# Kernel optimization log

Measured on AMD Instinct MI355X. Metric: run time of the kernel, lower is better.

The kernel has to match this reference:

```python
import jax, jax.numpy as jnp
import numpy as np

BATCH = 2048
SEQ_LEN = 8192


def setup_inputs() -> dict:
    key = jax.random.key(0)
    k1, k2 = jax.random.split(key)
    inputs = jax.random.normal(k1, (BATCH, SEQ_LEN), dtype=jnp.float32)
    filters = jax.random.normal(k2, (BATCH, SEQ_LEN), dtype=jnp.float32)
    return {"inputs": inputs, "filters": filters}


def reference(inputs, filters):
    # FFT-based long convolution with zero-padding to 2L (linear, not circular, conv).
    # torch norm='forward': rfft divides by n, irfft multiplies by n -> net scale 1/n.
    L = inputs.shape[-1]
    n = 2 * L  # rfft with n=2L implicitly zero-pads, same as F.pad then rfft
    x_f = jnp.fft.rfft(inputs, n=n, axis=-1, norm="forward")   # (B, L+1) complex
    h_f = jnp.fft.rfft(filters, n=n, axis=-1, norm="forward")  # (B, L+1) complex
    y = jnp.fft.irfft(x_f * h_f, n=n, axis=-1, norm="forward")  # (B, 2L)
    return y[..., :L]
```

## Files before the change

kernel.cpp:

```cpp
#include <hip/hip_runtime.h>

#define L_LEN 8192
#define N_FFT 16384
#define NB    1024

#define LB __launch_bounds__(NB)

typedef float f2 __attribute__((ext_vector_type(2)));

__device__ __forceinline__ f2 mkf2(float a, float b) { f2 v; v.x = a; v.y = b; return v; }

__device__ __forceinline__ f2 cmul(f2 a, f2 w) {
    return mkf2(a.y, a.y) * mkf2(-w.y, w.x) + mkf2(a.x, a.x) * w;
}

__device__ __forceinline__ void sincos_rev(float rev, float* sn, float* cs) {
    *sn = __builtin_amdgcn_sinf(rev);
    *cs = __builtin_amdgcn_cosf(rev);
}

__host__ __device__ constexpr int swz(int i) {
    return i ^ ((((i) >> 4) ^ ((i) >> 8) ^ ((i) >> 12)) & 15);
}

__device__ __forceinline__ int rev4_12(int m) {
    int r = 0;
#pragma unroll
    for (int d = 0; d < 6; ++d) { r = (r << 2) | (m & 3); m >>= 2; }
    return r;
}

__device__ __forceinline__ void bfly_dif(f2& x0, f2& x1, f2& x2, f2& x3,
                                         f2 w1, f2 w2, f2 w3) {
    f2 A = x0 + x2, B = x0 - x2, C = x1 + x3, D = x1 - x3;
    f2 iD = mkf2(-D.y, D.x);
    x0 = A + C;
    x1 = cmul(B - iD, w1);
    x2 = cmul(A - C, w2);
    x3 = cmul(B + iD, w3);
}

__device__ __forceinline__ void bfly_dit(f2& x0, f2& x1, f2& x2, f2& x3,
                                         f2 w1, f2 w2, f2 w3) {
    f2 a1 = cmul(x1, w1), a2 = cmul(x2, w2), a3 = cmul(x3, w3);
    f2 E = x0 + a2, F = x0 - a2, G = a1 + a3, K = a1 - a3;
    f2 iK = mkf2(-K.y, K.x);
    x0 = E + G; x1 = F + iK; x2 = E - G; x3 = F - iK;
}

__device__ __forceinline__ void bfly_dif1(f2* z) {
    f2 A = z[0] + z[2], B = z[0] - z[2], C = z[1] + z[3], D = z[1] - z[3];
    f2 iD = mkf2(-D.y, D.x);
    z[0] = A + C; z[1] = B - iD; z[2] = A - C; z[3] = B + iD;
}
__device__ __forceinline__ void bfly_dit1(f2* z) {
    f2 E = z[0] + z[2], F = z[0] - z[2], G = z[1] + z[3], K = z[1] - z[3];
    f2 iK = mkf2(-K.y, K.x);
    z[0] = E + G; z[1] = F + iK; z[2] = E - G; z[3] = F - iK;
}

__device__ __forceinline__ void pointwise_pair(f2& Zm, f2& Zr) {
    f2 half = mkf2(0.5f, 0.5f);
    f2 X = half * (Zm + mkf2(Zr.x, -Zr.y));
    f2 H = half * (mkf2(Zm.y, -Zm.x) + mkf2(Zr.y, Zr.x));
    f2 Y = cmul(X, H);
    Zm = Y;
    Zr = mkf2(Y.x, -Y.y);
}

#define CT0 1.0f
#define CT1 0.92387953251128674f
#define CT2 0.70710678118654752f
#define CT3 0.38268343236508977f
#define ST1 0.38268343236508977f
#define ST2 0.70710678118654752f
#define ST3 0.92387953251128674f

__device__ __forceinline__ void fwd_first(f2* lds, int tid,
                                          const float* __restrict__ xr,
                                          const float* __restrict__ hr) {
    f2 r[4][4];
    float snA, csA;
    sincos_rev((float)tid * (-1.0f / 16384.f), &snA, &csA);
    f2 u1 = mkf2(csA, snA);
    const f2 lad[4] = {mkf2(CT0, 0.f), mkf2(CT1, -ST1), mkf2(CT2, -ST2), mkf2(CT3, -ST3)};
#pragma unroll
    for (int jB = 0; jB < 4; ++jB) {
        const int t = tid + jB * 1024;
        f2 z0 = mkf2(xr[t], hr[t]);
        f2 z1 = mkf2(xr[t + 4096], hr[t + 4096]);
        f2 w1 = (jB == 0) ? u1 : cmul(u1, lad[jB]);
        f2 w2 = cmul(w1, w1);
        f2 w3 = cmul(w2, w1);
        f2 iz1 = mkf2(-z1.y, z1.x);
        r[0][jB] = z0 + z1;
        r[1][jB] = cmul(z0 - iz1, w1);
        r[2][jB] = cmul(z0 - z1, w2);
        r[3][jB] = cmul(z0 + iz1, w3);
    }
    float sn, cs;
    sincos_rev((float)tid * (-1.0f / 4096.f), &sn, &cs);
    f2 v1 = mkf2(cs, sn);
    f2 v2 = cmul(v1, v1);
    f2 v3 = cmul(v2, v1);
#pragma unroll
    for (int jA = 0; jA < 4; ++jA)
        bfly_dif(r[jA][0], r[jA][1], r[jA][2], r[jA][3], v1, v2, v3);

    const int sb = swz(tid);
#pragma unroll
    for (int jA = 0; jA < 4; ++jA)
#pragma unroll
        for (int jB = 0; jB < 4; ++jB)
            lds[sb ^ swz(jA * 4096 + jB * 1024)] = r[jA][jB];
}

__device__ __forceinline__ void inv_last(const f2* lds, int tid,
                                         float* __restrict__ orow) {
    const int sb = swz(tid);
    f2 r[4][4];
#pragma unroll
    for (int jA = 0; jA < 4; ++jA)
#pragma unroll
        for (int jB = 0; jB < 4; ++jB)
            r[jA][jB] = lds[sb ^ swz(jA * 1024 + jB * 4096)];

    {
        float sn, cs;
        sincos_rev((float)tid * (1.0f / 4096.f), &sn, &cs);
        f2 a1 = mkf2(cs, sn);
        f2 a2 = cmul(a1, a1);
        f2 a3 = cmul(a2, a1);
#pragma unroll
        for (int jB = 0; jB < 4; ++jB)
            bfly_dit(r[0][jB], r[1][jB], r[2][jB], r[3][jB], a1, a2, a3);
    }
    const float scale = 1.0f / ((float)N_FFT * (float)N_FFT);
    float sn, cs;
    sincos_rev((float)tid * (1.0f / 16384.f), &sn, &cs);
    f2 b1 = mkf2(cs, sn);
    const f2 lad[4] = {mkf2(CT0, 0.f), mkf2(CT1, ST1), mkf2(CT2, ST2), mkf2(CT3, ST3)};
#pragma unroll
    for (int jA = 0; jA < 4; ++jA) {
        f2 w1 = (jA == 0) ? b1 : cmul(b1, lad[jA]);
        f2 w2 = cmul(w1, w1);
        f2 w3 = cmul(w2, w1);
        f2 x0 = r[jA][0];
        f2 a1 = cmul(r[jA][1], w1);
        f2 a2 = cmul(r[jA][2], w2);
        f2 a3 = cmul(r[jA][3], w3);
        float y0 = x0.x + a2.x + a1.x + a3.x;
        float y1 = x0.x - a2.x - a1.y + a3.y;
        orow[tid + jA * 1024]        = y0 * scale;
        orow[tid + jA * 1024 + 4096] = y1 * scale;
    }
}

template<int QA>
__device__ __forceinline__ void fwd_pair(f2* lds, int tid) {
    constexpr int QB = QA / 4;
    const int g = tid / QB;
    const int u = tid % QB;
    const int sb = swz(g * (4 * QA) + u);
    f2 r[4][4];
#pragma unroll
    for (int jA = 0; jA < 4; ++jA)
#pragma unroll
        for (int jB = 0; jB < 4; ++jB)
            r[jA][jB] = lds[sb ^ swz(jA * QA + jB * QB)];

    {
        float sn, cs;
        sincos_rev((float)u * (-1.0f / (float)(4 * QA)), &sn, &cs);
        f2 u1 = mkf2(cs, sn);
        const f2 lad[4] = {mkf2(CT0, 0.f), mkf2(CT1, -ST1), mkf2(CT2, -ST2), mkf2(CT3, -ST3)};
#pragma unroll
        for (int jB = 0; jB < 4; ++jB) {
            f2 w1 = (jB == 0) ? u1 : cmul(u1, lad[jB]);
            f2 w2 = cmul(w1, w1);
            f2 w3 = cmul(w2, w1);
            bfly_dif(r[0][jB], r[1][jB], r[2][jB], r[3][jB], w1, w2, w3);
        }
    }
    {
        float sn, cs;
        sincos_rev((float)u * (-1.0f / (float)(4 * QB)), &sn, &cs);
        f2 v1 = mkf2(cs, sn);
        f2 v2 = cmul(v1, v1);
        f2 v3 = cmul(v2, v1);
#pragma unroll
        for (int jA = 0; jA < 4; ++jA)
            bfly_dif(r[jA][0], r[jA][1], r[jA][2], r[jA][3], v1, v2, v3);
    }

#pragma unroll
    for (int jA = 0; jA < 4; ++jA)
#pragma unroll
        for (int jB = 0; jB < 4; ++jB)
            lds[sb ^ swz(jA * QA + jB * QB)] = r[jA][jB];
}

template<int QA>
__device__ __forceinline__ void inv_pair(f2* lds, int tid) {
    constexpr int QB = 4 * QA;
    const int G = tid / QA;
    const int u = tid % QA;
    const int sb = swz(G * (16 * QA) + u);
    f2 r[4][4];
#pragma unroll
    for (int jA = 0; jA < 4; ++jA)
#pragma unroll
        for (int jB = 0; jB < 4; ++jB)
            r[jA][jB] = lds[sb ^ swz(jA * QA + jB * QB)];

    {
        float sn, cs;
        sincos_rev((float)u * (1.0f / (float)(4 * QA)), &sn, &cs);
        f2 a1 = mkf2(cs, sn);
        f2 a2 = cmul(a1, a1);
        f2 a3 = cmul(a2, a1);
#pragma unroll
        for (int jB = 0; jB < 4; ++jB)
            bfly_dit(r[0][jB], r[1][jB], r[2][jB], r[3][jB], a1, a2, a3);
    }
    {
        float sn, cs;
        sincos_rev((float)u * (1.0f / (float)(4 * QB)), &sn, &cs);
        f2 b1 = mkf2(cs, sn);
        const f2 lad[4] = {mkf2(CT0, 0.f), mkf2(CT1, ST1), mkf2(CT2, ST2), mkf2(CT3, ST3)};
#pragma unroll
        for (int jA = 0; jA < 4; ++jA) {
            f2 w1 = (jA == 0) ? b1 : cmul(b1, lad[jA]);
            f2 w2 = cmul(w1, w1);
            f2 w3 = cmul(w2, w1);
            bfly_dit(r[jA][0], r[jA][1], r[jA][2], r[jA][3], w1, w2, w3);
        }
    }

#pragma unroll
    for (int jA = 0; jA < 4; ++jA)
#pragma unroll
        for (int jB = 0; jB < 4; ++jB)
            lds[sb ^ swz(jA * QA + jB * QB)] = r[jA][jB];
}

__global__ LB
void fftconv_kernel(const float* __restrict__ xin,
                    const float* __restrict__ hin,
                    float* __restrict__ out)
{
    __shared__ f2 lds[N_FFT];

    const int row = blockIdx.x;
    const int tid = threadIdx.x;
    const float* xr = xin + (size_t)row * L_LEN;
    const float* hr = hin + (size_t)row * L_LEN;

    fwd_first(lds, tid, xr, hr);
    __syncthreads();

    fwd_pair<256>(lds, tid);
    asm volatile("" ::: "memory");
    fwd_pair<16>(lds, tid);
    __syncthreads();

#pragma unroll
    for (int iter = 0; iter < 2; ++iter) {
        const int p = tid + iter * NB;
        if (p == 0) {
            f2 z[4];
#pragma unroll
            for (int k = 0; k < 4; ++k) z[k] = lds[k];
            bfly_dif1(z);
            z[0] = mkf2(z[0].x * z[0].y, 0.f);
            z[2] = mkf2(z[2].x * z[2].y, 0.f);
            pointwise_pair(z[1], z[3]);
            bfly_dit1(z);
#pragma unroll
            for (int k = 0; k < 4; ++k) lds[k] = z[k];
            f2 w[4];
#pragma unroll
            for (int k = 0; k < 4; ++k) w[k] = lds[8 + k];
            bfly_dif1(w);
            pointwise_pair(w[0], w[3]);
            pointwise_pair(w[1], w[2]);
            bfly_dit1(w);
#pragma unroll
            for (int k = 0; k < 4; ++k) lds[8 + k] = w[k];
        } else {
            const int sA = swz(4 * rev4_12(p));
            const int sB = swz(4 * rev4_12(4096 - p));
            f2 A[4], B[4];
#pragma unroll
            for (int k = 0; k < 4; ++k) A[k] = lds[sA ^ k];
#pragma unroll
            for (int k = 0; k < 4; ++k) B[k] = lds[sB ^ k];
            bfly_dif1(A);
            bfly_dif1(B);
            pointwise_pair(A[0], B[3]);
            pointwise_pair(A[1], B[2]);
            pointwise_pair(A[2], B[1]);
            pointwise_pair(A[3], B[0]);
            bfly_dit1(A);
            bfly_dit1(B);
#pragma unroll
            for (int k = 0; k < 4; ++k) lds[sA ^ k] = A[k];
#pragma unroll
            for (int k = 0; k < 4; ++k) lds[sB ^ k] = B[k];
        }
    }
    __syncthreads();

    inv_pair<4>(lds, tid);
    asm volatile("" ::: "memory");
    inv_pair<64>(lds, tid);
    __syncthreads();

    inv_last(lds, tid, out + (size_t)row * L_LEN);
}

extern "C" void kernel_launch(void* const* d_in, const int* in_sizes, int n_in,
                              void* d_out, int out_size, void* d_ws, size_t ws_size,
                              hipStream_t stream) {
    const float* x = (const float*)d_in[0];
    const float* h = (const float*)d_in[1];
    float* out = (float*)d_out;
    const int rows = in_sizes[0] / L_LEN;
    fftconv_kernel<<<dim3(rows), dim3(NB), 0, stream>>>(x, h, out);
}
```

Baseline: 112.2 us.

## Use half-length complex inverse FFT via real-output packing

Replaces the full 16384-point complex inverse FFT with a real-to-complex packing trick. The pointwise spectrum product is folded into an 8192-point complex spectrum that produces only the needed first L real outputs. The inverse passes then run as two 4096-point halves on 512 threads, and the last stage writes paired float2 outputs. This cuts inverse butterfly work and LDS traffic, but half the threads sit idle during the inverse stages and an extra barrier is added.

```diff
diff --git a/kernel.cpp b/kernel.cpp
--- a/kernel.cpp
+++ b/kernel.cpp
@@ -18,12 +18,15 @@
     *sn = __builtin_amdgcn_sinf(rev);
     *cs = __builtin_amdgcn_cosf(rev);
 }
+__device__ __forceinline__ f2 cis_rev(float rev) {
+    return mkf2(__builtin_amdgcn_cosf(rev), __builtin_amdgcn_sinf(rev));
+}
 
 __host__ __device__ constexpr int swz(int i) {
     return i ^ ((((i) >> 4) ^ ((i) >> 8) ^ ((i) >> 12)) & 15);
 }
 
-__device__ __forceinline__ int rev4_12(int m) {
+__device__ __forceinline__ int rev6(int m) {
     int r = 0;
 #pragma unroll
     for (int d = 0; d < 6; ++d) { r = (r << 2) | (m & 3); m >>= 2; }
@@ -53,19 +56,12 @@
     f2 iD = mkf2(-D.y, D.x);
     z[0] = A + C; z[1] = B - iD; z[2] = A - C; z[3] = B + iD;
 }
-__device__ __forceinline__ void bfly_dit1(f2* z) {
-    f2 E = z[0] + z[2], F = z[0] - z[2], G = z[1] + z[3], K = z[1] - z[3];
-    f2 iK = mkf2(-K.y, K.x);
-    z[0] = E + G; z[1] = F + iK; z[2] = E - G; z[3] = F - iK;
-}
-
-__device__ __forceinline__ void pointwise_pair(f2& Zm, f2& Zr) {
+
+__device__ __forceinline__ f2 pwY(f2 Zm, f2 Zr) {
     f2 half = mkf2(0.5f, 0.5f);
     f2 X = half * (Zm + mkf2(Zr.x, -Zr.y));
     f2 H = half * (mkf2(Zm.y, -Zm.x) + mkf2(Zr.y, Zr.x));
-    f2 Y = cmul(X, H);
-    Zm = Y;
-    Zr = mkf2(Y.x, -Y.y);
+    return cmul(X, H);
 }
 
 #define CT0 1.0f
@@ -115,47 +111,6 @@
             lds[sb ^ swz(jA * 4096 + jB * 1024)] = r[jA][jB];
 }
 
-__device__ __forceinline__ void inv_last(const f2* lds, int tid,
-                                         float* __restrict__ orow) {
-    const int sb = swz(tid);
-    f2 r[4][4];
-#pragma unroll
-    for (int jA = 0; jA < 4; ++jA)
-#pragma unroll
-        for (int jB = 0; jB < 4; ++jB)
-            r[jA][jB] = lds[sb ^ swz(jA * 1024 + jB * 4096)];
-
-    {
-        float sn, cs;
-        sincos_rev((float)tid * (1.0f / 4096.f), &sn, &cs);
-        f2 a1 = mkf2(cs, sn);
-        f2 a2 = cmul(a1, a1);
-        f2 a3 = cmul(a2, a1);
-#pragma unroll
-        for (int jB = 0; jB < 4; ++jB)
-            bfly_dit(r[0][jB], r[1][jB], r[2][jB], r[3][jB], a1, a2, a3);
-    }
-    const float scale = 1.0f / ((float)N_FFT * (float)N_FFT);
-    float sn, cs;
-    sincos_rev((float)tid * (1.0f / 16384.f), &sn, &cs);
-    f2 b1 = mkf2(cs, sn);
-    const f2 lad[4] = {mkf2(CT0, 0.f), mkf2(CT1, ST1), mkf2(CT2, ST2), mkf2(CT3, ST3)};
-#pragma unroll
-    for (int jA = 0; jA < 4; ++jA) {
-        f2 w1 = (jA == 0) ? b1 : cmul(b1, lad[jA]);
-        f2 w2 = cmul(w1, w1);
-        f2 w3 = cmul(w2, w1);
-        f2 x0 = r[jA][0];
-        f2 a1 = cmul(r[jA][1], w1);
-        f2 a2 = cmul(r[jA][2], w2);
-        f2 a3 = cmul(r[jA][3], w3);
-        float y0 = x0.x + a2.x + a1.x + a3.x;
-        float y1 = x0.x - a2.x - a1.y + a3.y;
-        orow[tid + jA * 1024]        = y0 * scale;
-        orow[tid + jA * 1024 + 4096] = y1 * scale;
-    }
-}
-
 template<int QA>
 __device__ __forceinline__ void fwd_pair(f2* lds, int tid) {
     constexpr int QB = QA / 4;
@@ -200,12 +155,72 @@
             lds[sb ^ swz(jA * QA + jB * QB)] = r[jA][jB];
 }
 
+__device__ __forceinline__ void combo_item(const f2* lds, int b, f2* Zi, int* sl) {
+    const int sA = swz(4 * rev6(b));
+    const int sB = swz(4 * rev6(4096 - b));
+    f2 A[4], B[4];
+#pragma unroll
+    for (int k = 0; k < 4; ++k) { A[k] = lds[sA ^ k]; B[k] = lds[sB ^ k]; }
+    bfly_dif1(A);
+    bfly_dif1(B);
+    f2 Yb   = pwY(A[0], B[3]);
+    f2 Yb4  = pwY(A[1], B[2]);
+    f2 Yb8  = pwY(A[2], B[1]);
+    f2 Yb12 = pwY(A[3], B[0]);
+    f2 t = cis_rev((float)b * (1.0f / 16384.f));
+    f2 S  = Yb + Yb8,   D  = Yb - Yb8;
+    f2 Sp = Yb4 + Yb12, Dp = Yb4 - Yb12;
+    f2 c  = cmul(D, t);
+    f2 cp = cmul(Dp, t);
+    Zi[0] = mkf2(S.x - c.y,    S.y + c.x);
+    Zi[1] = Sp - cp;
+    Zi[2] = mkf2(Sp.x + cp.x, -(Sp.y + cp.y));
+    Zi[3] = mkf2(S.x + c.y,   -S.y + c.x);
+    const int sbase = (b & 1) ? 4097 : 0;
+    const int ra = rev6(b >> 1);
+    const int rc = rev6((4096 - b) >> 1);
+    sl[0] = sbase ^ swz(ra);
+    sl[1] = sl[0] ^ 2;
+    sl[2] = sbase ^ swz(rc);
+    sl[3] = sl[2] ^ 2;
+}
+
+__device__ __forceinline__ void combo_special(const f2* lds, f2* Zi, int* sl) {
+    f2 z[4];
+#pragma unroll
+    for (int k = 0; k < 4; ++k) z[k] = lds[k];
+    bfly_dif1(z);
+    float Y0 = z[0].x * z[0].y;
+    float Y8 = z[2].x * z[2].y;
+    f2 Y4096 = pwY(z[1], z[3]);
+    Zi[0] = mkf2(Y0 + Y8, Y0 - Y8);          sl[0] = 0;
+    Zi[1] = mkf2(2.f * Y4096.x, -2.f * Y4096.y); sl[1] = 2;
+    f2 w[4];
+#pragma unroll
+    for (int k = 0; k < 4; ++k) w[k] = lds[8 + k];
+    bfly_dif1(w);
+    f2 Y2048 = pwY(w[0], w[3]);
+    f2 Y6144 = pwY(w[1], w[2]);
+    f2 cj6 = mkf2(Y6144.x, -Y6144.y);
+    f2 S1 = Y2048 + cj6, D1 = Y2048 - cj6;
+    f2 t1 = mkf2(0.70710678118654752f, 0.70710678118654752f);
+    f2 c1 = cmul(D1, t1);
+    Zi[2] = mkf2(S1.x - c1.y, S1.y + c1.x);  sl[2] = 1;
+    f2 cj2 = mkf2(Y2048.x, -Y2048.y);
+    f2 S2 = Y6144 + cj2, D2 = Y6144 - cj2;
+    f2 t2 = mkf2(-0.70710678118654752f, 0.70710678118654752f);
+    f2 c2 = cmul(D2, t2);
+    Zi[3] = mkf2(S2.x - c2.y, S2.y + c2.x);  sl[3] = 3;
+}
+
 template<int QA>
-__device__ __forceinline__ void inv_pair(f2* lds, int tid) {
+__device__ __forceinline__ void inv_half(f2* lds, int th) {
     constexpr int QB = 4 * QA;
-    const int G = tid / QA;
-    const int u = tid % QA;
-    const int sb = swz(G * (16 * QA) + u);
+    const int h = th >> 8;
+    const int k = th & 255;
+    const int g = k / QA, u = k % QA;
+    const int base = g * (16 * QA) + u;
+    const int sb = (h ? 4097 : 0) ^ swz(base);
     f2 r[4][4];
 #pragma unroll
     for (int jA = 0; jA < 4; ++jA)
@@ -214,34 +229,46 @@
             r[jA][jB] = lds[sb ^ swz(jA * QA + jB * QB)];
 
     {
-        float sn, cs;
-        sincos_rev((float)u * (1.0f / (float)(4 * QA)), &sn, &cs);
-        f2 a1 = mkf2(cs, sn);
-        f2 a2 = cmul(a1, a1);
-        f2 a3 = cmul(a2, a1);
+        f2 a1;
+        if constexpr (QA == 1) a1 = mkf2(1.f, 0.f);
+        else { float sn, cs; sincos_rev((float)u * (1.0f / (float)(4 * QA)), &sn, &cs); a1 = mkf2(cs, sn); }
+        f2 a2 = cmul(a1, a1), a3 = cmul(a2, a1);
 #pragma unroll
         for (int jB = 0; jB < 4; ++jB)
             bfly_dit(r[0][jB], r[1][jB], r[2][jB], r[3][jB], a1, a2, a3);
     }
     {
-        float sn, cs;
-        sincos_rev((float)u * (1.0f / (float)(4 * QB)), &sn, &cs);
-        f2 b1 = mkf2(cs, sn);
+        f2 b1;
+        if constexpr (QA == 1) b1 = mkf2(1.f, 0.f);
+        else { float sn, cs; sincos_rev((float)u * (1.0f / (float)(16 * QA)), &sn, &cs); b1 = mkf2(cs, sn); }
         const f2 lad[4] = {mkf2(CT0, 0.f), mkf2(CT1, ST1), mkf2(CT2, ST2), mkf2(CT3, ST3)};
 #pragma unroll
         for (int jA = 0; jA < 4; ++jA) {
             f2 w1 = (jA == 0) ? b1 : cmul(b1, lad[jA]);
-            f2 w2 = cmul(w1, w1);
-            f2 w3 = cmul(w2, w1);
+            f2 w2 = cmul(w1, w1), w3 = cmul(w2, w1);
             bfly_dit(r[jA][0], r[jA][1], r[jA][2], r[jA][3], w1, w2, w3);
         }
     }
-
 #pragma unroll
     for (int jA = 0; jA < 4; ++jA)
 #pragma unroll
         for (int jB = 0; jB < 4; ++jB)
             lds[sb ^ swz(jA * QA + jB * QB)] = r[jA][jB];
+}
+
+__device__ __forceinline__ void inv_last(const f2* lds, int tid,
+                                         float* __restrict__ orow) {
+    const float sc = 1.0f / (16384.f * 16384.f);
+#pragma unroll
+    for (int i = 0; i < 4; ++i) {
+        const int m = tid + i * 1024;
+        const int sm = swz(m);
+        f2 P = lds[sm];
+        f2 Q = lds[sm ^ 4097];
+        f2 t = cis_rev((float)m * (1.0f / 8192.f));
+        f2 w = P + cmul(Q, t);
+        *(f2*)(orow + 2 * m) = mkf2(w.x * sc, w.y * sc);
+    }
 }
 
 __global__ LB
@@ -258,62 +285,30 @@
 
     fwd_first(lds, tid, xr, hr);
     __syncthreads();
-
     fwd_pair<256>(lds, tid);
     asm volatile("" ::: "memory");
     fwd_pair<16>(lds, tid);
     __syncthreads();
 
-#pragma unroll
-    for (int iter = 0; iter < 2; ++iter) {
-        const int p = tid + iter * NB;
-        if (p == 0) {
-            f2 z[4];
-#pragma unroll
-            for (int k = 0; k < 4; ++k) z[k] = lds[k];
-            bfly_dif1(z);
-            z[0] = mkf2(z[0].x * z[0].y, 0.f);
-            z[2] = mkf2(z[2].x * z[2].y, 0.f);
-            pointwise_pair(z[1], z[3]);
-            bfly_dit1(z);
-#pragma unroll
-            for (int k = 0; k < 4; ++k) lds[k] = z[k];
-            f2 w[4];
-#pragma unroll
-            for (int k = 0; k < 4; ++k) w[k] = lds[8 + k];
-            bfly_dif1(w);
-            pointwise_pair(w[0], w[3]);
-            pointwise_pair(w[1], w[2]);
-            bfly_dit1(w);
-#pragma unroll
-            for (int k = 0; k < 4; ++k) lds[8 + k] = w[k];
-        } else {
-            const int sA = swz(4 * rev4_12(p));
-            const int sB = swz(4 * rev4_12(4096 - p));
-            f2 A[4], B[4];
-#pragma unroll
-            for (int k = 0; k < 4; ++k) A[k] = lds[sA ^ k];
-#pragma unroll
-            for (int k = 0; k < 4; ++k) B[k] = lds[sB ^ k];
-            bfly_dif1(A);
-            bfly_dif1(B);
-            pointwise_pair(A[0], B[3]);
-            pointwise_pair(A[1], B[2]);
-            pointwise_pair(A[2], B[1]);
-            pointwise_pair(A[3], B[0]);
-            bfly_dit1(A);
-            bfly_dit1(B);
-#pragma unroll
-            for (int k = 0; k < 4; ++k) lds[sA ^ k] = A[k];
-#pragma unroll
-            for (int k = 0; k < 4; ++k) lds[sB ^ k] = B[k];
-        }
-    }
-    __syncthreads();
-
-    inv_pair<4>(lds, tid);
-    asm volatile("" ::: "memory");
-    inv_pair<64>(lds, tid);
+    {
+        f2 Zi0[4], Zi1[4];
+        int s0[4], s1[4];
+        if (tid == 0) combo_special(lds, Zi0, s0);
+        else          combo_item(lds, tid, Zi0, s0);
+        combo_item(lds, tid + 1024, Zi1, s1);
+        __syncthreads();
+#pragma unroll
+        for (int k = 0; k < 4; ++k) { lds[s0[k]] = Zi0[k]; lds[s1[k]] = Zi1[k]; }
+    }
+    __syncthreads();
+
+    if (tid < 512) {
+        inv_half<1>(lds, tid);
+        asm volatile("" ::: "memory");
+        inv_half<16>(lds, tid);
+    }
+    __syncthreads();
+    if (tid < 512) inv_half<256>(lds, tid);
     __syncthreads();
 
     inv_last(lds, tid, out + (size_t)row * L_LEN);
```

Measured after the change: 107.5 us, median of 2. 1.04x faster.
